# Kernel tuning notes

Hardware: AMD Instinct MI355X
Metric: run time of the kernel (lower is better)

The kernel has to match this reference:

```python
import jax, jax.numpy as jnp
import numpy as np

B, T, D, H = 8, 512, 1024, 16
DK = D // H          # 64
S = 2 * T - 1        # 1023 relative positions


def setup_inputs() -> dict:
    key = jax.random.key(0)
    ks = jax.random.split(key, 10)
    s = 0.02
    return {
        "x": jax.random.normal(ks[0], (B, T, D), jnp.float32),
        "mask": jax.random.randint(ks[1], (B, T, T), 0, 2) > 0,
        "pos": jax.random.normal(ks[2], (1, S, D), jnp.float32),
        "Wqkv": jax.random.normal(ks[3], (3 * D, D), jnp.float32) * s,
        "bqkv": jnp.zeros((3 * D,), jnp.float32),
        "Wpos": jax.random.normal(ks[4], (D, D), jnp.float32) * s,
        "posu": jax.random.normal(ks[5], (1, 1, H, DK), jnp.float32) * s,
        "posv": jax.random.normal(ks[6], (1, 1, H, DK), jnp.float32) * s,
        "Wout": jax.random.normal(ks[7], (D, D), jnp.float32) * s,
        "bout": jnp.zeros((D,), jnp.float32),
    }


def reference(x, mask, pos, Wqkv, bqkv, Wpos, posu, posv, Wout, bout):
    # QKV projection and head split
    qkv = x @ Wqkv.T + bqkv                               # [B,T,3D]
    q, k, v = jnp.split(qkv, 3, axis=-1)
    q = q.reshape(B, T, H, DK)                            # [B,T,H,dk]
    k = k.reshape(B, T, H, DK).transpose(0, 2, 1, 3)      # [B,H,T,dk]
    v = v.reshape(B, T, H, DK).transpose(0, 2, 1, 3)      # [B,H,T,dk]
    # positional projection (no bias)
    p = (pos @ Wpos.T).reshape(1, S, H, DK).transpose(0, 2, 1, 3)  # [1,H,S,dk]
    # content (AC) and position (BD) terms
    q_u = (q + posu).transpose(0, 2, 1, 3)                # [B,H,T,dk]
    q_v = (q + posv).transpose(0, 2, 1, 3)                # [B,H,T,dk]
    AC = jnp.einsum('bhtd,bhsd->bhts', q_u, k)            # [B,H,T,T]
    matrix_bd = jnp.einsum('bhtd,zhsd->bhts', q_v, p)     # [B,H,T,S]
    # Transformer-XL style relative gather: index (j - i) + (T-1)
    r = jnp.arange(T)
    rel = (r[None, :] - r[:, None]) + (T - 1)             # [T,T], values in [0, S)
    BD = jnp.take_along_axis(matrix_bd, rel[None, None], axis=3)  # [B,H,T,T]
    scores = (AC + BD) / jnp.sqrt(jnp.float32(DK))
    scores = jnp.where(mask[:, None], scores, jnp.float32(-100000.0))
    weights = jax.nn.softmax(scores, axis=-1)             # [B,H,T,T]
    ctx = jnp.einsum('bhts,bhsd->bthd', weights, v).reshape(B, T, D)
    out = ctx @ Wout.T + bout                             # dropout rate 0 -> identity
    return out, weights
```

## Files before the change

kernel.cpp:

```cpp
#include <hip/hip_runtime.h>

#define BB 8
#define TT 512
#define DD 1024
#define HH 16
#define DKK 64
#define SS 1023

typedef unsigned short u16;
typedef __attribute__((ext_vector_type(8))) short bf16x8;
typedef __attribute__((ext_vector_type(4))) float f32x4;

#define MFMA16(a, b, c) __builtin_amdgcn_mfma_f32_16x16x32_bf16((a), (b), (c), 0, 0, 0)

#define WAVE_SYNC() do { asm volatile("s_waitcnt lgkmcnt(0)" ::: "memory"); __builtin_amdgcn_sched_barrier(0); } while (0)

__device__ __forceinline__ float us2f(u16 u) {
    unsigned int x = ((unsigned int)u) << 16;
    return __uint_as_float(x);
}
__device__ __forceinline__ u16 f2us(float f) {
    unsigned int x = __float_as_uint(f);
    unsigned int lsb = (x >> 16) & 1u;
    x += 0x7fffu + lsb;
    return (u16)(x >> 16);
}
__device__ __forceinline__ bf16x8 cvt8(const float* p) {
    float4 f1 = *(const float4*)p;
    float4 f2 = *(const float4*)(p + 4);
    bf16x8 r;
    r[0] = (short)f2us(f1.x); r[1] = (short)f2us(f1.y);
    r[2] = (short)f2us(f1.z); r[3] = (short)f2us(f1.w);
    r[4] = (short)f2us(f2.x); r[5] = (short)f2us(f2.y);
    r[6] = (short)f2us(f2.z); r[7] = (short)f2us(f2.w);
    return r;
}

__global__ void detect_kernel(const u16* __restrict__ w,
                              const unsigned int* __restrict__ mask,
                              int* __restrict__ flags) {
    if (threadIdx.x == 0 && blockIdx.x == 0) {
        int plaus = 0;
        for (int i = 0; i < 256; i++) {
            u16 hw = w[i];
            int e = (hw >> 7) & 0xFF;
            if (e == 0 || (e >= 87 && e <= 131)) plaus++;
        }
        flags[0] = (plaus >= 205) ? 1 : 0;
        int ok = 1;
        for (int i = 0; i < 64; i++) if (mask[i] > 1u) ok = 0;
        flags[1] = ok;
    }
}

__global__ __launch_bounds__(256) void pack_mask(const void* __restrict__ mask,
                                                 unsigned int* __restrict__ packed,
                                                 const int* __restrict__ flags) {
    const int idx = blockIdx.x * 256 + threadIdx.x;
    const int g = idx & 15;
    const size_t bt = (size_t)(idx >> 4);
    unsigned int bits = 0;
    if (flags[1]) {
        const int* mp = (const int*)mask + bt * TT + g;
        #pragma unroll
        for (int k = 0; k < 32; k++) if (mp[k * 16] != 0) bits |= (1u << k);
    } else {
        const signed char* mp = (const signed char*)mask + bt * TT + g;
        #pragma unroll
        for (int k = 0; k < 32; k++) if (mp[k * 16] != 0) bits |= (1u << k);
    }
    packed[idx] = bits;
}

template<int OMODE>
__global__ __launch_bounds__(256) void gemm_mfma(
    const void* __restrict__ Av, const void* __restrict__ Wv,
    const void* __restrict__ bias, const int* __restrict__ flags,
    float* __restrict__ qT, u16* __restrict__ kB, u16* __restrict__ vB,
    u16* __restrict__ pB, void* __restrict__ oout, int M, int N, int K)
{
    const bool isbf = (flags[0] != 0);
    __shared__ u16 As[64][40];
    __shared__ u16 Bs[64][40];
    const int tid = threadIdx.x;
    const int w = tid >> 6, lane = tid & 63;
    const int quad = lane >> 4, l16 = lane & 15;
    const int bn = blockIdx.x * 64, bm = blockIdx.y * 64;
    const int srow = tid >> 2;
    const int koff = (tid & 3) * 8;
    const int garow = (OMODE == 1) ? min(bm + srow, M - 1) : (bm + srow);
    const int gbrow = bn + srow;

    f32x4 C[4];
    #pragma unroll
    for (int i = 0; i < 4; i++) { C[i][0] = 0.f; C[i][1] = 0.f; C[i][2] = 0.f; C[i][3] = 0.f; }

    for (int k0 = 0; k0 < K; k0 += 32) {
        bf16x8 av, bv;
        if (OMODE == 2) {
            const int kk = k0 + koff;
            const float* ap = qT + (((size_t)((garow >> 9) * HH + (kk >> 6)) * TT + (garow & 511)) << 6) + (kk & 63);
            av = cvt8(ap);
        } else if (isbf) {
            av = *(const bf16x8*)((const u16*)Av + (size_t)garow * K + k0 + koff);
        } else {
            av = cvt8((const float*)Av + (size_t)garow * K + k0 + koff);
        }
        if (isbf) {
            bv = *(const bf16x8*)((const u16*)Wv + (size_t)gbrow * K + k0 + koff);
        } else {
            bv = cvt8((const float*)Wv + (size_t)gbrow * K + k0 + koff);
        }

        __syncthreads();
        *(bf16x8*)&As[srow][koff] = av;
        *(bf16x8*)&Bs[srow][koff] = bv;
        __syncthreads();

        bf16x8 af = *(const bf16x8*)&As[w * 16 + l16][quad * 8];
        #pragma unroll
        for (int ct = 0; ct < 4; ct++) {
            bf16x8 bf = *(const bf16x8*)&Bs[ct * 16 + l16][quad * 8];
            C[ct] = MFMA16(af, bf, C[ct]);
        }
    }

    #pragma unroll
    for (int ct = 0; ct < 4; ct++) {
        #pragma unroll
        for (int r = 0; r < 4; r++) {
            const int i = bm + w * 16 + quad * 4 + r;
            const int n = bn + ct * 16 + l16;
            float val = C[ct][r];
            if (OMODE == 0) {
                val += isbf ? us2f(((const u16*)bias)[n]) : ((const float*)bias)[n];
                const int sec = n >> 10, w_ = n & 1023;
                const int h_ = w_ >> 6, d_ = w_ & 63;
                const size_t bh_ = (size_t)((i >> 9) * HH + h_);
                const int t_ = i & 511;
                if (sec == 0) qT[((bh_ * TT + t_) << 6) + d_] = val;
                else if (sec == 1) kB[((bh_ * TT + t_) << 6) + d_] = f2us(val);
                else vB[((bh_ * DKK + d_) << 9) + t_] = f2us(val);
            } else if (OMODE == 1) {
                if (i < M) {
                    const int h_ = n >> 6, d_ = n & 63;
                    pB[((size_t)(h_ * 1024 + i) << 6) + d_] = f2us(val);
                }
            } else {
                val += isbf ? us2f(((const u16*)bias)[n]) : ((const float*)bias)[n];
                if (isbf) ((u16*)oout)[(size_t)i * N + n] = f2us(val);
                else ((float*)oout)[(size_t)i * N + n] = val;
            }
        }
    }
}

__global__ __launch_bounds__(256) void attn_mfma(
    float* __restrict__ qT, const u16* __restrict__ kB, const u16* __restrict__ vB,
    const u16* __restrict__ pB, const void* __restrict__ posu,
    const void* __restrict__ posv, const unsigned int* __restrict__ pmask,
    void* __restrict__ d_out, const int* __restrict__ flags)
{
    const int t0 = blockIdx.x << 6;
    const int h = blockIdx.y, b = blockIdx.z;
    const int tid = threadIdx.x;
    const int w = tid >> 6, lane = tid & 63;
    const int quad = lane >> 4, l16 = lane & 15;
    const bool isbf = (flags[0] != 0);
    const size_t bh = (size_t)b * HH + h;

    __shared__ u16 wls[4][16][520];
    u16* wme = &wls[w][0][0];
    float* bdw = (float*)wme;

    const int trow = t0 + w * 16 + quad * 4;
    unsigned int mrow[4];
    #pragma unroll
    for (int r = 0; r < 4; r++)
        mrow[r] = pmask[((size_t)(b * TT + trow + r) << 4) + l16];

    const int myrow = t0 + w * 16 + l16;
    const float* qrow = qT + ((bh * TT + myrow) << 6);
    bf16x8 aU[2], aV[2];
    #pragma unroll
    for (int f = 0; f < 2; f++) {
        const int d0 = f * 32 + quad * 8;
        float q8[8], pu8[8], pv8[8];
        *(float4*)&q8[0] = *(const float4*)(qrow + d0);
        *(float4*)&q8[4] = *(const float4*)(qrow + d0 + 4);
        if (isbf) {
            const u16* puP = (const u16*)posu + h * 64 + d0;
            const u16* pvP = (const u16*)posv + h * 64 + d0;
            #pragma unroll
            for (int j = 0; j < 8; j++) { pu8[j] = us2f(puP[j]); pv8[j] = us2f(pvP[j]); }
        } else {
            const float* puP = (const float*)posu + h * 64 + d0;
            const float* pvP = (const float*)posv + h * 64 + d0;
            #pragma unroll
            for (int j = 0; j < 8; j++) { pu8[j] = puP[j]; pv8[j] = pvP[j]; }
        }
        #pragma unroll
        for (int j = 0; j < 8; j++) {
            aU[f][j] = (short)f2us((q8[j] + pu8[j]) * 0.125f);
            aV[f][j] = (short)f2us((q8[j] + pv8[j]) * 0.125f);
        }
    }

    f32x4 S[32];
    #pragma unroll
    for (int ct = 0; ct < 32; ct++) { S[ct][0] = 0.f; S[ct][1] = 0.f; S[ct][2] = 0.f; S[ct][3] = 0.f; }
    const u16* kbase = kB + ((bh * TT) << 6) + quad * 8;
    #pragma unroll
    for (int ct = 0; ct < 32; ct++) {
        const u16* kp = kbase + ((size_t)(ct * 16 + l16) << 6);
        bf16x8 b0 = *(const bf16x8*)kp;
        bf16x8 b1 = *(const bf16x8*)(kp + 32);
        S[ct] = MFMA16(aU[0], b0, S[ct]);
        S[ct] = MFMA16(aU[1], b1, S[ct]);
    }

    const u16* pbaseh = pB + ((size_t)h << 16);
    for (int g = 0; g < 8; g++) {
        const int pb = g * 64 - t0 + 496 - w * 16;
        #pragma unroll
        for (int c5 = 0; c5 < 5; c5++) {
            const u16* pp = pbaseh + ((size_t)(pb + c5 * 16 + l16) << 6) + quad * 8;
            bf16x8 b0 = *(const bf16x8*)pp;
            bf16x8 b1 = *(const bf16x8*)(pp + 32);
            f32x4 c; c[0] = 0.f; c[1] = 0.f; c[2] = 0.f; c[3] = 0.f;
            c = MFMA16(aV[0], b0, c);
            c = MFMA16(aV[1], b1, c);
            #pragma unroll
            for (int r = 0; r < 4; r++)
                bdw[(quad * 4 + r) * 84 + c5 * 16 + l16] = c[r];
        }
        WAVE_SYNC();
        #pragma unroll
        for (int f = 0; f < 4; f++) {
            const int sc = f * 16 + l16;
            #pragma unroll
            for (int r = 0; r < 4; r++) {
                const int local = quad * 4 + r;
                S[g * 4 + f][r] += bdw[local * 83 + sc + 15];
            }
        }
    }

    #pragma unroll
    for (int ct = 0; ct < 32; ct++) {
        #pragma unroll
        for (int r = 0; r < 4; r++) {
            if (!(mrow[r] & (1u << ct))) S[ct][r] = -100000.0f;
        }
    }

    float mx[4] = {-3.0e38f, -3.0e38f, -3.0e38f, -3.0e38f};
    float sm[4] = {0.f, 0.f, 0.f, 0.f};
    #pragma unroll
    for (int ct = 0; ct < 32; ct++)
        #pragma unroll
        for (int r = 0; r < 4; r++) mx[r] = fmaxf(mx[r], S[ct][r]);
    #pragma unroll
    for (int r = 0; r < 4; r++)
        #pragma unroll
        for (int off = 1; off < 16; off <<= 1) mx[r] = fmaxf(mx[r], __shfl_xor(mx[r], off, 64));
    #pragma unroll
    for (int ct = 0; ct < 32; ct++)
        #pragma unroll
        for (int r = 0; r < 4; r++) {
            float e = __expf(S[ct][r] - mx[r]);
            S[ct][r] = e;
            sm[r] += e;
        }
    #pragma unroll
    for (int r = 0; r < 4; r++) {
        #pragma unroll
        for (int off = 1; off < 16; off <<= 1) sm[r] += __shfl_xor(sm[r], off, 64);
        sm[r] = 1.0f / sm[r];
    }

    const size_t wbase = (size_t)BB * TT * DD + (((bh * TT + trow)) << 9) + l16;
    #pragma unroll
    for (int ct = 0; ct < 32; ct++) {
        #pragma unroll
        for (int r = 0; r < 4; r++) {
            const float wv = S[ct][r] * sm[r];
            wls[w][quad * 4 + r][ct * 16 + l16] = f2us(wv);
            if (!isbf) ((float*)d_out)[wbase + ((size_t)r << 9) + ct * 16] = wv;
        }
    }
    WAVE_SYNC();
    if (isbf) {
        u16* wout = (u16*)d_out + (size_t)BB * TT * DD + ((bh * TT + t0 + w * 16) << 9);
        const int lane8 = lane * 8;
        #pragma unroll
        for (int rr = 0; rr < 16; rr++) {
            bf16x8 vv = *(const bf16x8*)&wls[w][rr][lane8];
            *(bf16x8*)(wout + ((size_t)rr << 9) + lane8) = vv;
        }
    }

    f32x4 Cv[4];
    #pragma unroll
    for (int i = 0; i < 4; i++) { Cv[i][0] = 0.f; Cv[i][1] = 0.f; Cv[i][2] = 0.f; Cv[i][3] = 0.f; }
    const u16* vb0 = vB + ((bh * DKK) << 9) + quad * 8;
    #pragma unroll
    for (int ks = 0; ks < 16; ks++) {
        bf16x8 aw = *(const bf16x8*)&wls[w][l16][ks * 32 + quad * 8];
        #pragma unroll
        for (int ctd = 0; ctd < 4; ctd++) {
            const u16* vp = vb0 + ((size_t)(ctd * 16 + l16) << 9) + ks * 32;
            bf16x8 bv = *(const bf16x8*)vp;
            Cv[ctd] = MFMA16(aw, bv, Cv[ctd]);
        }
    }
    float* crow = qT + ((bh * TT + trow) << 6) + l16;
    #pragma unroll
    for (int ctd = 0; ctd < 4; ctd++)
        #pragma unroll
        for (int r = 0; r < 4; r++)
            crow[(r << 6) + ctd * 16] = Cv[ctd][r];
}

extern "C" void kernel_launch(void* const* d_in, const int* in_sizes, int n_in,
                              void* d_out, int out_size, void* d_ws, size_t ws_size,
                              hipStream_t stream)
{
    const void* x    = d_in[0];
    const void* mask = d_in[1];
    const void* pos  = d_in[2];
    const void* Wqkv = d_in[3];
    const void* bqkv = d_in[4];
    const void* Wpos = d_in[5];
    const void* posu = d_in[6];
    const void* posv = d_in[7];
    const void* Wout = d_in[8];
    const void* bout = d_in[9];

    char* ws = (char*)d_ws;
    float* qT    = (float*)(ws + 0);
    u16*   kB    = (u16*)(ws + 16777216);
    u16*   vB    = (u16*)(ws + 25165824);
    u16*   pB    = (u16*)(ws + 33554432);
    int*   flags = (int*)(ws + 35651584);
    unsigned int* pmask = (unsigned int*)(ws + 35655680);

    detect_kernel<<<1, 64, 0, stream>>>((const u16*)Wqkv, (const unsigned int*)mask, flags);
    pack_mask<<<dim3(256), 256, 0, stream>>>(mask, pmask, flags);

    gemm_mfma<0><<<dim3(48, 64), 256, 0, stream>>>(
        x, Wqkv, bqkv, flags, qT, kB, vB, pB, nullptr, BB * TT, 3 * DD, DD);

    gemm_mfma<1><<<dim3(16, 16), 256, 0, stream>>>(
        pos, Wpos, nullptr, flags, qT, kB, vB, pB, nullptr, SS, DD, DD);

    attn_mfma<<<dim3(8, HH, BB), 256, 0, stream>>>(
        qT, kB, vB, pB, posu, posv, pmask, d_out, flags);

    gemm_mfma<2><<<dim3(16, 64), 256, 0, stream>>>(
        nullptr, Wout, bout, flags, qT, kB, vB, pB, d_out, BB * TT, DD, DD);
}
```

Baseline: 501.7 us.

## Enlarge GEMM tiles to 128x128 with 2x2 wave layout; nontemporal output stores

The shared GEMM kernel moves from 64x64 block tiles, where each wave computed a 16x64 strip, to 128x128 tiles with a 2x2 wave grid. Each wave now computes a 64x64 sub-tile with a 4x4 array of MFMA accumulators, and grids shrink to match. This raises operand reuse per LDS load and per global load. The output projection and the attention-weight writes switch to nontemporal stores so streaming output does not pollute cache. The price is fewer blocks (e.g. only 64 blocks for the positional GEMM), which lowers occupancy and CU fill on a large GPU, plus higher register use for the 64 accumulator floats.

```diff
diff --git a/kernel.cpp b/kernel.cpp
--- a/kernel.cpp
+++ b/kernel.cpp
@@ -80,79 +80,101 @@
     u16* __restrict__ pB, void* __restrict__ oout, int M, int N, int K)
 {
     const bool isbf = (flags[0] != 0);
-    __shared__ u16 As[64][40];
-    __shared__ u16 Bs[64][40];
+    __shared__ u16 As[128][40];
+    __shared__ u16 Bs[128][40];
     const int tid = threadIdx.x;
     const int w = tid >> 6, lane = tid & 63;
     const int quad = lane >> 4, l16 = lane & 15;
-    const int bn = blockIdx.x * 64, bm = blockIdx.y * 64;
-    const int srow = tid >> 2;
+    const int wr = w >> 1, wc = w & 1;
+    const int bn = blockIdx.x * 128, bm = blockIdx.y * 128;
+    const int r0 = tid >> 2;
     const int koff = (tid & 3) * 8;
-    const int garow = (OMODE == 1) ? min(bm + srow, M - 1) : (bm + srow);
-    const int gbrow = bn + srow;
-
-    f32x4 C[4];
-    #pragma unroll
-    for (int i = 0; i < 4; i++) { C[i][0] = 0.f; C[i][1] = 0.f; C[i][2] = 0.f; C[i][3] = 0.f; }
+
+    f32x4 acc[4][4];
+    #pragma unroll
+    for (int m = 0; m < 4; m++)
+        #pragma unroll
+        for (int n = 0; n < 4; n++) {
+            acc[m][n][0] = 0.f; acc[m][n][1] = 0.f;
+            acc[m][n][2] = 0.f; acc[m][n][3] = 0.f;
+        }
 
     for (int k0 = 0; k0 < K; k0 += 32) {
-        bf16x8 av, bv;
+        int ar0 = bm + r0, ar1 = bm + r0 + 64;
+        if (OMODE == 1) { ar0 = min(ar0, M - 1); ar1 = min(ar1, M - 1); }
+        const int br0 = bn + r0, br1 = bn + r0 + 64;
+
+        bf16x8 a0, a1, b0, b1;
         if (OMODE == 2) {
             const int kk = k0 + koff;
-            const float* ap = qT + (((size_t)((garow >> 9) * HH + (kk >> 6)) * TT + (garow & 511)) << 6) + (kk & 63);
-            av = cvt8(ap);
+            const float* ap0 = qT + (((size_t)((ar0 >> 9) * HH + (kk >> 6)) * TT + (ar0 & 511)) << 6) + (kk & 63);
+            const float* ap1 = qT + (((size_t)((ar1 >> 9) * HH + (kk >> 6)) * TT + (ar1 & 511)) << 6) + (kk & 63);
+            a0 = cvt8(ap0); a1 = cvt8(ap1);
         } else if (isbf) {
-            av = *(const bf16x8*)((const u16*)Av + (size_t)garow * K + k0 + koff);
+            a0 = *(const bf16x8*)((const u16*)Av + (size_t)ar0 * K + k0 + koff);
+            a1 = *(const bf16x8*)((const u16*)Av + (size_t)ar1 * K + k0 + koff);
         } else {
-            av = cvt8((const float*)Av + (size_t)garow * K + k0 + koff);
+            a0 = cvt8((const float*)Av + (size_t)ar0 * K + k0 + koff);
+            a1 = cvt8((const float*)Av + (size_t)ar1 * K + k0 + koff);
         }
         if (isbf) {
-            bv = *(const bf16x8*)((const u16*)Wv + (size_t)gbrow * K + k0 + koff);
+            b0 = *(const bf16x8*)((const u16*)Wv + (size_t)br0 * K + k0 + koff);
+            b1 = *(const bf16x8*)((const u16*)Wv + (size_t)br1 * K + k0 + koff);
         } else {
-            bv = cvt8((const float*)Wv + (size_t)gbrow * K + k0 + koff);
+            b0 = cvt8((const float*)Wv + (size_t)br0 * K + k0 + koff);
+            b1 = cvt8((const float*)Wv + (size_t)br1 * K + k0 + koff);
         }
 
         __syncthreads();
-        *(bf16x8*)&As[srow][koff] = av;
-        *(bf16x8*)&Bs[srow][koff] = bv;
+        *(bf16x8*)&As[r0][koff] = a0;
+        *(bf16x8*)&As[r0 + 64][koff] = a1;
+        *(bf16x8*)&Bs[r0][koff] = b0;
+        *(bf16x8*)&Bs[r0 + 64][koff] = b1;
         __syncthreads();
 
-        bf16x8 af = *(const bf16x8*)&As[w * 16 + l16][quad * 8];
-        #pragma unroll
-        for (int ct = 0; ct < 4; ct++) {
-            bf16x8 bf = *(const bf16x8*)&Bs[ct * 16 + l16][quad * 8];
-            C[ct] = MFMA16(af, bf, C[ct]);
-        }
-    }
-
-    #pragma unroll
-    for (int ct = 0; ct < 4; ct++) {
-        #pragma unroll
-        for (int r = 0; r < 4; r++) {
-            const int i = bm + w * 16 + quad * 4 + r;
-            const int n = bn + ct * 16 + l16;
-            float val = C[ct][r];
-            if (OMODE == 0) {
-                val += isbf ? us2f(((const u16*)bias)[n]) : ((const float*)bias)[n];
-                const int sec = n >> 10, w_ = n & 1023;
-                const int h_ = w_ >> 6, d_ = w_ & 63;
-                const size_t bh_ = (size_t)((i >> 9) * HH + h_);
-                const int t_ = i & 511;
-                if (sec == 0) qT[((bh_ * TT + t_) << 6) + d_] = val;
-                else if (sec == 1) kB[((bh_ * TT + t_) << 6) + d_] = f2us(val);
-                else vB[((bh_ * DKK + d_) << 9) + t_] = f2us(val);
-            } else if (OMODE == 1) {
-                if (i < M) {
-                    const int h_ = n >> 6, d_ = n & 63;
-                    pB[((size_t)(h_ * 1024 + i) << 6) + d_] = f2us(val);
+        bf16x8 af[4], bf[4];
+        #pragma unroll
+        for (int m = 0; m < 4; m++)
+            af[m] = *(const bf16x8*)&As[wr * 64 + m * 16 + l16][quad * 8];
+        #pragma unroll
+        for (int n = 0; n < 4; n++)
+            bf[n] = *(const bf16x8*)&Bs[wc * 64 + n * 16 + l16][quad * 8];
+        #pragma unroll
+        for (int m = 0; m < 4; m++)
+            #pragma unroll
+            for (int n = 0; n < 4; n++)
+                acc[m][n] = MFMA16(af[m], bf[n], acc[m][n]);
+    }
+
+    #pragma unroll
+    for (int m = 0; m < 4; m++)
+        #pragma unroll
+        for (int nn = 0; nn < 4; nn++)
+            #pragma unroll
+            for (int rr = 0; rr < 4; rr++) {
+                const int i = bm + wr * 64 + m * 16 + quad * 4 + rr;
+                const int n = bn + wc * 64 + nn * 16 + l16;
+                float val = acc[m][nn][rr];
+                if (OMODE == 0) {
+                    val += isbf ? us2f(((const u16*)bias)[n]) : ((const float*)bias)[n];
+                    const int sec = n >> 10, w_ = n & 1023;
+                    const int h_ = w_ >> 6, d_ = w_ & 63;
+                    const size_t bh_ = (size_t)((i >> 9) * HH + h_);
+                    const int t_ = i & 511;
+                    if (sec == 0) qT[((bh_ * TT + t_) << 6) + d_] = val;
+                    else if (sec == 1) kB[((bh_ * TT + t_) << 6) + d_] = f2us(val);
+                    else vB[((bh_ * DKK + d_) << 9) + t_] = f2us(val);
+                } else if (OMODE == 1) {
+                    if (i < M) {
+                        const int h_ = n >> 6, d_ = n & 63;
+                        pB[((size_t)(h_ * 1024 + i) << 6) + d_] = f2us(val);
+                    }
+                } else {
+                    val += isbf ? us2f(((const u16*)bias)[n]) : ((const float*)bias)[n];
+                    if (isbf) __builtin_nontemporal_store(f2us(val), &((u16*)oout)[(size_t)i * N + n]);
+                    else      __builtin_nontemporal_store(val, &((float*)oout)[(size_t)i * N + n]);
                 }
-            } else {
-                val += isbf ? us2f(((const u16*)bias)[n]) : ((const float*)bias)[n];
-                if (isbf) ((u16*)oout)[(size_t)i * N + n] = f2us(val);
-                else ((float*)oout)[(size_t)i * N + n] = val;
             }
-        }
-    }
 }
 
 __global__ __launch_bounds__(256) void attn_mfma(
@@ -286,7 +308,7 @@
         for (int r = 0; r < 4; r++) {
             const float wv = S[ct][r] * sm[r];
             wls[w][quad * 4 + r][ct * 16 + l16] = f2us(wv);
-            if (!isbf) ((float*)d_out)[wbase + ((size_t)r << 9) + ct * 16] = wv;
+            if (!isbf) __builtin_nontemporal_store(wv, &((float*)d_out)[wbase + ((size_t)r << 9) + ct * 16]);
         }
     }
     WAVE_SYNC();
@@ -296,7 +318,7 @@
         #pragma unroll
         for (int rr = 0; rr < 16; rr++) {
             bf16x8 vv = *(const bf16x8*)&wls[w][rr][lane8];
-            *(bf16x8*)(wout + ((size_t)rr << 9) + lane8) = vv;
+            __builtin_nontemporal_store(vv, (bf16x8*)(wout + ((size_t)rr << 9) + lane8));
         }
     }
 
@@ -348,15 +370,15 @@
     detect_kernel<<<1, 64, 0, stream>>>((const u16*)Wqkv, (const unsigned int*)mask, flags);
     pack_mask<<<dim3(256), 256, 0, stream>>>(mask, pmask, flags);
 
-    gemm_mfma<0><<<dim3(48, 64), 256, 0, stream>>>(
+    gemm_mfma<0><<<dim3(24, 32), 256, 0, stream>>>(
         x, Wqkv, bqkv, flags, qT, kB, vB, pB, nullptr, BB * TT, 3 * DD, DD);
 
-    gemm_mfma<1><<<dim3(16, 16), 256, 0, stream>>>(
+    gemm_mfma<1><<<dim3(8, 8), 256, 0, stream>>>(
         pos, Wpos, nullptr, flags, qT, kB, vB, pB, nullptr, SS, DD, DD);
 
     attn_mfma<<<dim3(8, HH, BB), 256, 0, stream>>>(
         qT, kB, vB, pB, posu, posv, pmask, d_out, flags);
 
-    gemm_mfma<2><<<dim3(16, 64), 256, 0, stream>>>(
+    gemm_mfma<2><<<dim3(8, 32), 256, 0, stream>>>(
         nullptr, Wout, bout, flags, qT, kB, vB, pB, d_out, BB * TT, DD, DD);
 }
```

New measurement: 513.5 us. 1.02x slower.
